# Performance work log

Hardware: AMD Instinct MI355X
Metric: run time of the kernel (lower is better)

## Reference

```python
import jax, jax.numpy as jnp
import numpy as np

N_NODES = 50000
N_EDGES = 1600000


def _glorot(key, shape):
    fan_in, fan_out = shape[-1], int(np.prod(shape[:-1]))
    limit = float(np.sqrt(6.0 / (fan_in + fan_out)))
    return jax.random.uniform(key, shape, jnp.float32, -limit, limit)


def setup_inputs() -> dict:
    key = jax.random.key(0)
    ks = jax.random.split(key, 10)
    x = jax.random.normal(ks[0], (N_NODES, 128), jnp.float32)
    edge_index = jax.random.randint(ks[1], (2, N_EDGES), 0, N_NODES, jnp.int64 if jax.config.jax_enable_x64 else jnp.int32)
    # Layer 1: in=128, heads=8, out=8 (concat -> 64)
    W1 = _glorot(ks[2], (8 * 8, 128))          # [H*F, F_in]
    a_src1 = _glorot(ks[3], (1, 8, 8))
    a_trg1 = _glorot(ks[4], (1, 8, 8))
    b1 = jnp.zeros((8 * 8,), jnp.float32)
    # Layer 2: in=64, heads=1, out=7 (mean -> 7)
    W2 = _glorot(ks[5], (1 * 7, 64))
    a_src2 = _glorot(ks[6], (1, 1, 7))
    a_trg2 = _glorot(ks[7], (1, 1, 7))
    b2 = jnp.zeros((7,), jnp.float32)
    return {"x": x, "edge_index": edge_index, "W1": W1, "a_src1": a_src1,
            "a_trg1": a_trg1, "b1": b1, "W2": W2, "a_src2": a_src2,
            "a_trg2": a_trg2, "b2": b2}


def _segment_softmax(scores, seg, num_segments):
    # scores: [E, H], seg: [E] target-node ids. Numerically-stable softmax per segment.
    m = jax.ops.segment_max(scores, seg, num_segments=num_segments)
    e = jnp.exp(scores - m[seg])
    s = jax.ops.segment_sum(e, seg, num_segments=num_segments)
    return e / (s[seg] + 1e-16)


def _gat_layer(x, edge_index, W, a_src, a_trg, bias, concat, activation):
    N = x.shape[0]
    H, F = a_src.shape[1], a_src.shape[2]
    proj = (x @ W.T).reshape(N, H, F)                 # [N, H, F]
    s_src = jnp.sum(proj * a_src, axis=-1)            # [N, H]
    s_trg = jnp.sum(proj * a_trg, axis=-1)            # [N, H]
    src, trg = edge_index[0], edge_index[1]
    scores = jax.nn.leaky_relu(s_src[src] + s_trg[trg], 0.2)   # [E, H]
    att = _segment_softmax(scores, trg, N)            # [E, H]
    msg = proj[src] * att[..., None]                  # [E, H, F]
    out = jax.ops.segment_sum(msg, trg, num_segments=N)  # [N, H, F]
    out = out.reshape(N, H * F) if concat else out.mean(axis=1)
    return activation(out + bias)


def reference(x, edge_index, W1, a_src1, a_trg1, b1, W2, a_src2, a_trg2, b2):
    # Dropout is identity at inference.
    h = _gat_layer(x, edge_index, W1, a_src1, a_trg1, b1, concat=True, activation=jax.nn.elu)
    out = _gat_layer(h, edge_index, W2, a_src2, a_trg2, b2, concat=False,
                     activation=lambda z: jax.nn.softmax(z, axis=-1))
    return out
```

## Files before the change

kernel.cpp:

```cpp
#include <hip/hip_runtime.h>
#include <hip/hip_fp16.h>
#include <math.h>


#define PAD 96
#define NRANGE 4

__device__ __forceinline__ float leaky02(float v){ return fmaxf(v, 0.2f*v); }

__device__ __forceinline__ int edge_lo(const void* ei, int isI32, long long idx){
  if (isI32) return ((const int*)ei)[idx];
  return ((const int*)ei)[2*idx];
}

__global__ void k_detect(const unsigned int* __restrict__ w, int nwords, int* __restrict__ flag){
  int gid = blockIdx.x*256 + threadIdx.x;
  int stride = gridDim.x*256;
  unsigned int v = 0;
  for (int idx = 2*gid + 1; idx < nwords; idx += 2*stride)
    v |= w[idx];
  unsigned long long b = __ballot(v != 0);
  if ((threadIdx.x & 63) == 0 && b != 0ULL) atomicOr(flag, 1);
}

__global__ __launch_bounds__(256) void k_build(
    const void* __restrict__ ei, const int* __restrict__ flag,
    int* __restrict__ cnt, unsigned short* __restrict__ padded,
    const float* __restrict__ x, const float* __restrict__ W,
    const float* __restrict__ a_src, const float* __restrict__ a_trg,
    __half* __restrict__ proj, float* __restrict__ s_src, float* __restrict__ s_trg,
    int E, int N, int nch, int gb){
  const int LP = 68;
  __shared__ float xsT[32*LP];
  __shared__ float wT [32*LP];

  if ((int)blockIdx.x < gb){
    int tid = threadIdx.x;
    int n0  = blockIdx.x*64;
    int tn = tid & 15, tm = tid >> 4;
    const float4* x4 = (const float4*)x;
    float acc[4][4] = {};

    for (int kq = 0; kq < 4; ++kq){
      __syncthreads();
      #pragma unroll
      for (int it=0; it<8; ++it){
        int idx = it*256 + tid;
        int c = idx >> 5, k = idx & 31;
        wT[k*LP + c] = W[c*128 + kq*32 + k];
      }
      #pragma unroll
      for (int it=0; it<2; ++it){
        int idx = it*256 + tid;
        int r = idx >> 3, k4 = idx & 7;
        int row = n0 + r;
        float4 v = (row < N) ? x4[(size_t)row*32 + kq*8 + k4] : make_float4(0.f,0.f,0.f,0.f);
        xsT[(k4*4+0)*LP + r] = v.x;
        xsT[(k4*4+1)*LP + r] = v.y;
        xsT[(k4*4+2)*LP + r] = v.z;
        xsT[(k4*4+3)*LP + r] = v.w;
      }
      __syncthreads();

      #pragma unroll 8
      for (int k=0; k<32; ++k){
        float4 av = *(const float4*)&xsT[k*LP + tm*4];
        float4 bv = *(const float4*)&wT [k*LP + tn*4];
        float a_[4] = {av.x, av.y, av.z, av.w};
        float b_[4] = {bv.x, bv.y, bv.z, bv.w};
        #pragma unroll
        for (int i=0;i<4;++i)
          #pragma unroll
          for (int j=0;j<4;++j)
            acc[i][j] += a_[i]*b_[j];
      }
    }

    float as[4], at[4];
    #pragma unroll
    for (int j=0;j<4;++j){ as[j] = a_src[tn*4+j]; at[j] = a_trg[tn*4+j]; }
    #pragma unroll
    for (int i=0;i<4;++i){
      int row = n0 + tm*4 + i;
      float ps = 0.f, pt = 0.f;
      #pragma unroll
      for (int j=0;j<4;++j){ ps += acc[i][j]*as[j]; pt += acc[i][j]*at[j]; }
      ps += __shfl_xor(ps, 1);
      pt += __shfl_xor(pt, 1);
      if (row < N){
        __half* pr = proj + (size_t)row*64 + tn*4;
        #pragma unroll
        for (int j=0;j<4;++j) pr[j] = __float2half(acc[i][j]);
        if ((tn & 1) == 0){
          s_src[row*8 + (tn>>1)] = ps;
          s_trg[row*8 + (tn>>1)] = pt;
        }
      }
    }
  } else {
    int sbid = (int)blockIdx.x - gb;
    int r  = sbid & (NRANGE-1);
    int c  = sbid / NRANGE;
    int lo = (int)((long long)E * c / nch);
    int hi = (int)((long long)E * (c+1) / nch);
    int rngw = (N + NRANGE-1) / NRANGE;
    int tlo = r * rngw, thi = min(tlo + rngw, N);
    int f = *flag;
    for (int e = lo + (int)threadIdx.x; e < hi; e += 256){
      int t = edge_lo(ei, f, (long long)e + E);
      t = min(max(t, 0), N-1);
      if (t < tlo || t >= thi) continue;
      int s = edge_lo(ei, f, (long long)e);
      s = min(max(s, 0), N-1);
      int slot = atomicAdd(&cnt[t], 1);
      if (slot < PAD) padded[(size_t)t*PAD + slot] = (unsigned short)s;
    }
  }
}

__global__ __launch_bounds__(64) void k_agg1f(
    const int* __restrict__ cnt, const unsigned short* __restrict__ padded,
    const float* __restrict__ ss, const float* __restrict__ st,
    const __half* __restrict__ proj, const float* __restrict__ b1,
    const float* __restrict__ W2, const float* __restrict__ as2, const float* __restrict__ at2,
    float* __restrict__ proj2, float* __restrict__ ssrc2, float* __restrict__ strg2, int N){
  int t = blockIdx.x;
  int lane = threadIdx.x;
  const unsigned short* srcs = padded + (size_t)t*PAD;
  int deg = min(cnt[t], PAD);

  int j = lane & 7;
  int h = lane >> 3;
  int k32 = lane & 31;
  int half = lane >> 5;
  int myhead = k32 >> 2;
  float sth = st[t*8 + h];

  float ax = 0.f, ay = 0.f;
  float dd  = 0.f;

  int e = 0;
  for (; e + 8 <= deg; e += 8){
    int sj = (int)srcs[e + j];
    float w = __expf(leaky02(ss[sj*8 + h] + sth));
    dd += w;
    #pragma unroll
    for (int i2 = 0; i2 < 4; ++i2){
      int jj   = 2*i2 + half;
      int sjj  = __shfl(sj, jj);
      float ww = __shfl(w, (myhead<<3) | jj);
      __half2 ph = *(const __half2*)&proj[(size_t)sjj*64 + 2*k32];
      float2 p2 = __half22float2(ph);
      ax += ww * p2.x;
      ay += ww * p2.y;
    }
  }
  for (; e < deg; ++e){
    int s0 = (int)srcs[e];
    float w0 = __expf(leaky02(ss[s0*8 + h] + sth));
    if (j == 0) dd += w0;
    float ww = __shfl(w0, myhead<<3);
    if (lane < 32){
      __half2 ph = *(const __half2*)&proj[(size_t)s0*64 + 2*k32];
      float2 p2 = __half22float2(ph);
      ax += ww * p2.x;
      ay += ww * p2.y;
    }
  }
  dd += __shfl_xor(dd, 1);
  dd += __shfl_xor(dd, 2);
  dd += __shfl_xor(dd, 4);

  ax += __shfl(ax, k32 + 32);
  ay += __shfl(ay, k32 + 32);

  float dh = __shfl(dd, myhead << 3);
  float rd = 1.f / (dh + 1e-16f);
  float zx = ax*rd + b1[2*k32];
  float zy = ay*rd + b1[2*k32+1];
  zx = (zx > 0.f) ? zx : expm1f(zx);
  zy = (zy > 0.f) ? zy : expm1f(zy);
  if (lane >= 32){ zx = 0.f; zy = 0.f; }

  float pf[7];
  #pragma unroll
  for (int f = 0; f < 7; ++f){
    float2 wv = *(const float2*)&W2[f*64 + 2*k32];
    float v = zx*wv.x + zy*wv.y;
    v += __shfl_xor(v, 1);
    v += __shfl_xor(v, 2);
    v += __shfl_xor(v, 4);
    v += __shfl_xor(v, 8);
    v += __shfl_xor(v, 16);
    v += __shfl_xor(v, 32);
    pf[f] = v;
  }
  if (lane == 0){
    float vs = 0.f, vt = 0.f;
    #pragma unroll
    for (int f = 0; f < 7; ++f){
      proj2[(size_t)t*8 + f] = pf[f];
      vs += pf[f] * as2[f];
      vt += pf[f] * at2[f];
    }
    proj2[(size_t)t*8 + 7] = 0.f;
    ssrc2[t] = vs;
    strg2[t] = vt;
  }
}

__global__ __launch_bounds__(64) void k_agg2(
    const int* __restrict__ cnt, const unsigned short* __restrict__ padded,
    const float* __restrict__ ss, const float* __restrict__ st,
    const float* __restrict__ proj2, const float* __restrict__ b2,
    float* __restrict__ out, int N){
  int t = blockIdx.x;
  int lane = threadIdx.x;
  const unsigned short* srcs = padded + (size_t)t*PAD;
  int deg = min(cnt[t], PAD);
  float stv = st[t];

  int f = lane & 7, g = lane >> 3;
  float a0 = 0.f, a1 = 0.f, d0 = 0.f, d1 = 0.f;
  int e = g;
  for (; e + 8 < deg; e += 16){
    int s0 = (int)srcs[e];
    int s1 = (int)srcs[e+8];
    float w0 = __expf(leaky02(ss[s0] + stv));
    float w1 = __expf(leaky02(ss[s1] + stv));
    a0 += w0 * proj2[(size_t)s0*8 + f]; d0 += w0;
    a1 += w1 * proj2[(size_t)s1*8 + f]; d1 += w1;
  }
  if (e < deg){
    int s0 = (int)srcs[e];
    float w0 = __expf(leaky02(ss[s0] + stv));
    a0 += w0 * proj2[(size_t)s0*8 + f]; d0 += w0;
  }
  float acc = a0 + a1, den = d0 + d1;
  acc += __shfl_xor(acc, 8);  den += __shfl_xor(den, 8);
  acc += __shfl_xor(acc, 16); den += __shfl_xor(den, 16);
  acc += __shfl_xor(acc, 32); den += __shfl_xor(den, 32);

  float z = (f < 7) ? acc / (den + 1e-16f) + b2[f] : -3.0e38f;
  float m = z;
  m = fmaxf(m, __shfl_xor(m, 1));
  m = fmaxf(m, __shfl_xor(m, 2));
  m = fmaxf(m, __shfl_xor(m, 4));
  float ev = (f < 7) ? __expf(z - m) : 0.f;
  float sum = ev;
  sum += __shfl_xor(sum, 1);
  sum += __shfl_xor(sum, 2);
  sum += __shfl_xor(sum, 4);
  if (lane < 7) out[(size_t)t*7 + lane] = ev / sum;
}

extern "C" void kernel_launch(void* const* d_in, const int* in_sizes, int n_in,
                              void* d_out, int out_size, void* d_ws, size_t ws_size,
                              hipStream_t stream){
  int N = in_sizes[0] / 128;
  int E = in_sizes[1] / 2;
  const float* x   = (const float*)d_in[0];
  const void*  ei  = d_in[1];
  const float* W1  = (const float*)d_in[2];
  const float* as1 = (const float*)d_in[3];
  const float* at1 = (const float*)d_in[4];
  const float* b1  = (const float*)d_in[5];
  const float* W2  = (const float*)d_in[6];
  const float* as2 = (const float*)d_in[7];
  const float* at2 = (const float*)d_in[8];
  const float* b2  = (const float*)d_in[9];
  float* out = (float*)d_out;

  auto aln = [](size_t v){ return (v + 255) & ~(size_t)255; };
  char* w = (char*)d_ws;
  int* flag              = (int*)w;            w += aln(4);
  int* cnt               = (int*)w;            w += aln((size_t)N*4);
  unsigned short* padded = (unsigned short*)w; w += aln((size_t)N*PAD*2);
  __half* proj1          = (__half*)w;         w += aln((size_t)N*64*2);
  float* ssrc1           = (float*)w;          w += aln((size_t)N*8*4);
  float* strg1           = (float*)w;          w += aln((size_t)N*8*4);
  float* proj2           = (float*)w;          w += aln((size_t)N*8*4);
  float* ssrc2           = (float*)w;          w += aln((size_t)N*4);
  float* strg2           = (float*)w;          w += aln((size_t)N*4);

  hipMemsetAsync(flag, 0, 4, stream);
  hipMemsetAsync(cnt, 0, (size_t)N*4, stream);

  int nch = 512;
  int SC  = nch*NRANGE;
  int GB  = (N + 63) / 64;
  int dwords = min(2*E, 1 << 21);

  k_detect<<<64, 256, 0, stream>>>((const unsigned int*)ei, dwords, flag);
  k_build <<<GB + SC, 256, 0, stream>>>(ei, flag, cnt, padded,
                                        x, W1, as1, at1, proj1, ssrc1, strg1,
                                        E, N, nch, GB);
  k_agg1f<<<N, 64, 0, stream>>>(cnt, padded, ssrc1, strg1, proj1, b1,
                                W2, as2, at2, proj2, ssrc2, strg2, N);
  k_agg2 <<<N, 64, 0, stream>>>(cnt, padded, ssrc2, strg2, proj2, b2, out, N);
}
```

Measured before the change: 185.4 us.

## Fold count zeroing into detect kernel, pack four nodes per block, store proj2 in fp16

The memset that cleared the per-node edge counters is replaced by a zeroing loop inside the detect kernel, removing one launch. Both aggregation kernels now handle four target nodes per 256-thread block instead of one per 64-thread block, which cuts the block count and scheduling overhead. The layer-2 projection buffer is stored in half precision, halving the bytes read during gathers at the cost of some accuracy. Any early return must stay wavefront-uniform, which it does here since t is computed per wave.

```diff
diff --git a/kernel.cpp b/kernel.cpp
--- a/kernel.cpp
+++ b/kernel.cpp
@@ -13,9 +13,11 @@
   return ((const int*)ei)[2*idx];
 }
 
-__global__ void k_detect(const unsigned int* __restrict__ w, int nwords, int* __restrict__ flag){
+__global__ void k_detect(const unsigned int* __restrict__ w, int nwords, int* __restrict__ flag,
+                         int* __restrict__ cnt, int N){
   int gid = blockIdx.x*256 + threadIdx.x;
   int stride = gridDim.x*256;
+  for (int i = gid; i < N; i += stride) cnt[i] = 0;
   unsigned int v = 0;
   for (int idx = 2*gid + 1; idx < nwords; idx += 2*stride)
     v |= w[idx];
@@ -118,14 +120,15 @@
   }
 }
 
-__global__ __launch_bounds__(64) void k_agg1f(
+__global__ __launch_bounds__(256) void k_agg1f(
     const int* __restrict__ cnt, const unsigned short* __restrict__ padded,
     const float* __restrict__ ss, const float* __restrict__ st,
     const __half* __restrict__ proj, const float* __restrict__ b1,
     const float* __restrict__ W2, const float* __restrict__ as2, const float* __restrict__ at2,
-    float* __restrict__ proj2, float* __restrict__ ssrc2, float* __restrict__ strg2, int N){
-  int t = blockIdx.x;
-  int lane = threadIdx.x;
+    __half* __restrict__ proj2, float* __restrict__ ssrc2, float* __restrict__ strg2, int N){
+  int t = blockIdx.x*4 + (threadIdx.x >> 6);
+  if (t >= N) return;
+  int lane = threadIdx.x & 63;
   const unsigned short* srcs = padded + (size_t)t*PAD;
   int deg = min(cnt[t], PAD);
 
@@ -199,23 +202,24 @@
     float vs = 0.f, vt = 0.f;
     #pragma unroll
     for (int f = 0; f < 7; ++f){
-      proj2[(size_t)t*8 + f] = pf[f];
+      proj2[(size_t)t*8 + f] = __float2half(pf[f]);
       vs += pf[f] * as2[f];
       vt += pf[f] * at2[f];
     }
-    proj2[(size_t)t*8 + 7] = 0.f;
+    proj2[(size_t)t*8 + 7] = __float2half(0.f);
     ssrc2[t] = vs;
     strg2[t] = vt;
   }
 }
 
-__global__ __launch_bounds__(64) void k_agg2(
+__global__ __launch_bounds__(256) void k_agg2(
     const int* __restrict__ cnt, const unsigned short* __restrict__ padded,
     const float* __restrict__ ss, const float* __restrict__ st,
-    const float* __restrict__ proj2, const float* __restrict__ b2,
+    const __half* __restrict__ proj2, const float* __restrict__ b2,
     float* __restrict__ out, int N){
-  int t = blockIdx.x;
-  int lane = threadIdx.x;
+  int t = blockIdx.x*4 + (threadIdx.x >> 6);
+  if (t >= N) return;
+  int lane = threadIdx.x & 63;
   const unsigned short* srcs = padded + (size_t)t*PAD;
   int deg = min(cnt[t], PAD);
   float stv = st[t];
@@ -228,13 +232,13 @@
     int s1 = (int)srcs[e+8];
     float w0 = __expf(leaky02(ss[s0] + stv));
     float w1 = __expf(leaky02(ss[s1] + stv));
-    a0 += w0 * proj2[(size_t)s0*8 + f]; d0 += w0;
-    a1 += w1 * proj2[(size_t)s1*8 + f]; d1 += w1;
+    a0 += w0 * __half2float(proj2[(size_t)s0*8 + f]); d0 += w0;
+    a1 += w1 * __half2float(proj2[(size_t)s1*8 + f]); d1 += w1;
   }
   if (e < deg){
     int s0 = (int)srcs[e];
     float w0 = __expf(leaky02(ss[s0] + stv));
-    a0 += w0 * proj2[(size_t)s0*8 + f]; d0 += w0;
+    a0 += w0 * __half2float(proj2[(size_t)s0*8 + f]); d0 += w0;
   }
   float acc = a0 + a1, den = d0 + d1;
   acc += __shfl_xor(acc, 8);  den += __shfl_xor(den, 8);
@@ -279,23 +283,22 @@
   __half* proj1          = (__half*)w;         w += aln((size_t)N*64*2);
   float* ssrc1           = (float*)w;          w += aln((size_t)N*8*4);
   float* strg1           = (float*)w;          w += aln((size_t)N*8*4);
-  float* proj2           = (float*)w;          w += aln((size_t)N*8*4);
+  __half* proj2          = (__half*)w;         w += aln((size_t)N*8*2);
   float* ssrc2           = (float*)w;          w += aln((size_t)N*4);
   float* strg2           = (float*)w;          w += aln((size_t)N*4);
 
   hipMemsetAsync(flag, 0, 4, stream);
-  hipMemsetAsync(cnt, 0, (size_t)N*4, stream);
 
   int nch = 512;
   int SC  = nch*NRANGE;
   int GB  = (N + 63) / 64;
   int dwords = min(2*E, 1 << 21);
 
-  k_detect<<<64, 256, 0, stream>>>((const unsigned int*)ei, dwords, flag);
+  k_detect<<<64, 256, 0, stream>>>((const unsigned int*)ei, dwords, flag, cnt, N);
   k_build <<<GB + SC, 256, 0, stream>>>(ei, flag, cnt, padded,
                                         x, W1, as1, at1, proj1, ssrc1, strg1,
                                         E, N, nch, GB);
-  k_agg1f<<<N, 64, 0, stream>>>(cnt, padded, ssrc1, strg1, proj1, b1,
-                                W2, as2, at2, proj2, ssrc2, strg2, N);
-  k_agg2 <<<N, 64, 0, stream>>>(cnt, padded, ssrc2, strg2, proj2, b2, out, N);
-}
+  k_agg1f<<<(N+3)/4, 256, 0, stream>>>(cnt, padded, ssrc1, strg1, proj1, b1,
+                                       W2, as2, at2, proj2, ssrc2, strg2, N);
+  k_agg2 <<<(N+3)/4, 256, 0, stream>>>(cnt, padded, ssrc2, strg2, proj2, b2, out, N);
+}
```

After: 190.0 us. +2.5%, slower.
